# Optimization experiments

Hardware: AMD Instinct MI355X
Metric: run time of the kernel (lower is better)

## Reference

```python
import jax, jax.numpy as jnp
import numpy as np


def setup_inputs() -> dict:
    key = jax.random.key(0)
    k1, k2 = jax.random.split(key)
    B, S, D = 4, 8192, 1024
    x = jax.random.normal(k1, (B, S, D), dtype=jnp.float32)
    alpha = jax.random.uniform(k2, (B, S, D), dtype=jnp.float32)
    return {"x": x, "alpha": alpha}


def reference(x, alpha):
    # Linear recurrence h_t = alpha_t * h_{t-1} + x_t, computed as an
    # associative scan over the sequence axis (axis=1).
    def linear_combine(i, j):
        x_i, a_i = i
        x_j, a_j = j
        return (a_j * x_i + x_j, a_j * a_i)

    ys, _ = jax.lax.associative_scan(linear_combine, (x, alpha), axis=1)
    return ys
```

## Files before the change

### kernel.cpp

```cpp
#include <hip/hip_runtime.h>

constexpr int B    = 4;
constexpr int S    = 8192;
constexpr int D    = 1024;
constexpr int CB   = 64;
constexpr int L    = S / CB;
constexpr int D4   = D / 4;
constexpr int NBLK = B * CB;
constexpr int G    = 8;
constexpr int NG   = L / G;

typedef float nt_float4 __attribute__((ext_vector_type(4)));

__device__ __forceinline__ void ast(float* p, float v) {
    __hip_atomic_store(p, v, __ATOMIC_RELAXED, __HIP_MEMORY_SCOPE_AGENT);
}
__device__ __forceinline__ float ald(const float* p) {
    return __hip_atomic_load(p, __ATOMIC_RELAXED, __HIP_MEMORY_SCOPE_AGENT);
}

__device__ __forceinline__ void gridbar(int* bar) {
    __syncthreads();
    if (threadIdx.x == 0) {
        __hip_atomic_fetch_add(bar, 1, __ATOMIC_ACQ_REL, __HIP_MEMORY_SCOPE_AGENT);
        while (__hip_atomic_load(bar, __ATOMIC_RELAXED, __HIP_MEMORY_SCOPE_AGENT) < NBLK)
            __builtin_amdgcn_s_sleep(2);
        __threadfence();
    }
    __syncthreads();
}

__device__ __forceinline__ void issue_grp(const float4* __restrict__ x,
                                          const float4* __restrict__ a,
                                          long o, float4 (&bx)[G], float4 (&ba)[G]) {
    #pragma unroll
    for (int j = 0; j < G; ++j) {
        bx[j] = x[o + (long)j * D4];
        ba[j] = a[o + (long)j * D4];
    }
}

__global__ __launch_bounds__(256, 1) void scan_coop(const float4* __restrict__ x,
                                                    const float4* __restrict__ a,
                                                    float4* __restrict__ out,
                                                    float* __restrict__ Xagg,
                                                    float* __restrict__ Aagg,
                                                    float* __restrict__ Pref,
                                                    int* __restrict__ bars) {
    const int t   = threadIdx.x;
    const int bid = blockIdx.x;
    const int b   = bid >> 6;
    const int c   = bid & (CB - 1);
    const long base = ((long)(b * S + c * L)) * D4 + t;

    float4 bx0[G], ba0[G], bx1[G], ba1[G];

    float4 X = {0.f, 0.f, 0.f, 0.f};
    float4 A = {1.f, 1.f, 1.f, 1.f};
    issue_grp(x, a, base, bx0, ba0);
    #pragma unroll
    for (int g = 0; g < NG; g += 2) {
        issue_grp(x, a, base + (long)(g + 1) * G * D4, bx1, ba1);
        #pragma unroll
        for (int j = 0; j < G; ++j) {
            X.x = fmaf(ba0[j].x, X.x, bx0[j].x); A.x *= ba0[j].x;
            X.y = fmaf(ba0[j].y, X.y, bx0[j].y); A.y *= ba0[j].y;
            X.z = fmaf(ba0[j].z, X.z, bx0[j].z); A.z *= ba0[j].z;
            X.w = fmaf(ba0[j].w, X.w, bx0[j].w); A.w *= ba0[j].w;
        }
        if (g + 2 < NG) issue_grp(x, a, base + (long)(g + 2) * G * D4, bx0, ba0);
        #pragma unroll
        for (int j = 0; j < G; ++j) {
            X.x = fmaf(ba1[j].x, X.x, bx1[j].x); A.x *= ba1[j].x;
            X.y = fmaf(ba1[j].y, X.y, bx1[j].y); A.y *= ba1[j].y;
            X.z = fmaf(ba1[j].z, X.z, bx1[j].z); A.z *= ba1[j].z;
            X.w = fmaf(ba1[j].w, X.w, bx1[j].w); A.w *= ba1[j].w;
        }
    }
    {
        float* Xp = Xagg + (long)bid * D + 4 * t;
        float* Ap = Aagg + (long)bid * D + 4 * t;
        ast(Xp + 0, X.x); ast(Xp + 1, X.y); ast(Xp + 2, X.z); ast(Xp + 3, X.w);
        ast(Ap + 0, A.x); ast(Ap + 1, A.y); ast(Ap + 2, A.z); ast(Ap + 3, A.w);
    }

    gridbar(bars + 0);

    if (bid < 16) {
        const int gg = bid * 256 + t;
        const int sb = gg >> 10;
        const int d  = gg & (D - 1);
        const float* Xp = Xagg + (long)sb * CB * D + d;
        const float* Ap = Aagg + (long)sb * CB * D + d;
        float*       Pp = Pref + (long)sb * CB * D + d;
        float carry = 0.f;
        for (int cc = 0; cc < CB; cc += 8) {
            float xv[8], av[8];
            #pragma unroll
            for (int j = 0; j < 8; ++j) {
                xv[j] = ald(Xp + (long)(cc + j) * D);
                av[j] = ald(Ap + (long)(cc + j) * D);
            }
            #pragma unroll
            for (int j = 0; j < 8; ++j) {
                ast(Pp + (long)(cc + j) * D, carry);
                carry = fmaf(av[j], carry, xv[j]);
            }
        }
    }

    gridbar(bars + 1);

    float4 h;
    {
        const float* Pp = Pref + (long)bid * D + 4 * t;
        h.x = ald(Pp + 0); h.y = ald(Pp + 1); h.z = ald(Pp + 2); h.w = ald(Pp + 3);
    }
    nt_float4* ntout = (nt_float4*)out;
    issue_grp(x, a, base, bx0, ba0);
    #pragma unroll
    for (int g = 0; g < NG; g += 2) {
        issue_grp(x, a, base + (long)(g + 1) * G * D4, bx1, ba1);
        #pragma unroll
        for (int j = 0; j < G; ++j) {
            h.x = fmaf(ba0[j].x, h.x, bx0[j].x);
            h.y = fmaf(ba0[j].y, h.y, bx0[j].y);
            h.z = fmaf(ba0[j].z, h.z, bx0[j].z);
            h.w = fmaf(ba0[j].w, h.w, bx0[j].w);
            nt_float4 hv = {h.x, h.y, h.z, h.w};
            __builtin_nontemporal_store(hv, &ntout[base + (long)(g * G + j) * D4]);
        }
        if (g + 2 < NG) issue_grp(x, a, base + (long)(g + 2) * G * D4, bx0, ba0);
        #pragma unroll
        for (int j = 0; j < G; ++j) {
            h.x = fmaf(ba1[j].x, h.x, bx1[j].x);
            h.y = fmaf(ba1[j].y, h.y, bx1[j].y);
            h.z = fmaf(ba1[j].z, h.z, bx1[j].z);
            h.w = fmaf(ba1[j].w, h.w, bx1[j].w);
            nt_float4 hv = {h.x, h.y, h.z, h.w};
            __builtin_nontemporal_store(hv, &ntout[base + (long)((g + 1) * G + j) * D4]);
        }
    }
}

extern "C" void kernel_launch(void* const* d_in, const int* in_sizes, int n_in,
                              void* d_out, int out_size, void* d_ws, size_t ws_size,
                              hipStream_t stream) {
    const float4* x = (const float4*)d_in[0];
    const float4* a = (const float4*)d_in[1];
    float4* out = (float4*)d_out;

    char* ws = (char*)d_ws;
    int*   bars = (int*)ws;
    float* Xagg = (float*)(ws + 4096);
    float* Aagg = Xagg + (size_t)NBLK * D;
    float* Pref = Aagg + (size_t)NBLK * D;

    hipMemsetAsync(ws, 0, 4096, stream);
    scan_coop<<<dim3(NBLK), 256, 0, stream>>>(x, a, out, Xagg, Aagg, Pref, bars);
}
```

Measured before the change: 430.2 us.

## Split each block's chunk into two half-chunks scanned by two thread teams

```diff
diff --git a/kernel.cpp b/kernel.cpp
--- a/kernel.cpp
+++ b/kernel.cpp
@@ -5,10 +5,11 @@
 constexpr int D    = 1024;
 constexpr int CB   = 64;
 constexpr int L    = S / CB;
+constexpr int HL   = L / 2;
 constexpr int D4   = D / 4;
 constexpr int NBLK = B * CB;
 constexpr int G    = 8;
-constexpr int NG   = L / G;
+constexpr int NG   = HL / G;
 
 typedef float nt_float4 __attribute__((ext_vector_type(4)));
 
@@ -40,18 +41,22 @@
     }
 }
 
-__global__ __launch_bounds__(256, 1) void scan_coop(const float4* __restrict__ x,
+__global__ __launch_bounds__(512, 1) void scan_coop(const float4* __restrict__ x,
                                                     const float4* __restrict__ a,
                                                     float4* __restrict__ out,
                                                     float* __restrict__ Xagg,
                                                     float* __restrict__ Aagg,
                                                     float* __restrict__ Pref,
                                                     int* __restrict__ bars) {
-    const int t   = threadIdx.x;
-    const int bid = blockIdx.x;
-    const int b   = bid >> 6;
-    const int c   = bid & (CB - 1);
-    const long base = ((long)(b * S + c * L)) * D4 + t;
+    const int t    = threadIdx.x;
+    const int team = t >> 8;
+    const int u    = t & 255;
+    const int bid  = blockIdx.x;
+    const int b    = bid >> 6;
+    const int c    = bid & (CB - 1);
+    const long base = ((long)(b * S + c * L + team * HL)) * D4 + u;
+
+    __shared__ float4 lX0[256], lA0[256];
 
     float4 bx0[G], ba0[G], bx1[G], ba1[G];
 
@@ -77,16 +82,24 @@
             X.w = fmaf(ba1[j].w, X.w, bx1[j].w); A.w *= ba1[j].w;
         }
     }
-    {
-        float* Xp = Xagg + (long)bid * D + 4 * t;
-        float* Ap = Aagg + (long)bid * D + 4 * t;
-        ast(Xp + 0, X.x); ast(Xp + 1, X.y); ast(Xp + 2, X.z); ast(Xp + 3, X.w);
-        ast(Ap + 0, A.x); ast(Ap + 1, A.y); ast(Ap + 2, A.z); ast(Ap + 3, A.w);
+    if (team == 0) { lX0[u] = X; lA0[u] = A; }
+    __syncthreads();
+    if (team == 1) {
+        const float4 X0 = lX0[u], A0 = lA0[u];
+        float4 Xc, Ac;
+        Xc.x = fmaf(A.x, X0.x, X.x); Ac.x = A.x * A0.x;
+        Xc.y = fmaf(A.y, X0.y, X.y); Ac.y = A.y * A0.y;
+        Xc.z = fmaf(A.z, X0.z, X.z); Ac.z = A.z * A0.z;
+        Xc.w = fmaf(A.w, X0.w, X.w); Ac.w = A.w * A0.w;
+        float* Xp = Xagg + (long)bid * D + 4 * u;
+        float* Ap = Aagg + (long)bid * D + 4 * u;
+        ast(Xp + 0, Xc.x); ast(Xp + 1, Xc.y); ast(Xp + 2, Xc.z); ast(Xp + 3, Xc.w);
+        ast(Ap + 0, Ac.x); ast(Ap + 1, Ac.y); ast(Ap + 2, Ac.z); ast(Ap + 3, Ac.w);
     }
 
     gridbar(bars + 0);
 
-    if (bid < 16) {
+    if (bid < 16 && t < 256) {
         const int gg = bid * 256 + t;
         const int sb = gg >> 10;
         const int d  = gg & (D - 1);
@@ -113,8 +126,16 @@
 
     float4 h;
     {
-        const float* Pp = Pref + (long)bid * D + 4 * t;
-        h.x = ald(Pp + 0); h.y = ald(Pp + 1); h.z = ald(Pp + 2); h.w = ald(Pp + 3);
+        const float* Pp = Pref + (long)bid * D + 4 * u;
+        float4 cb;
+        cb.x = ald(Pp + 0); cb.y = ald(Pp + 1); cb.z = ald(Pp + 2); cb.w = ald(Pp + 3);
+        if (team == 0) h = cb;
+        else {
+            h.x = fmaf(lA0[u].x, cb.x, lX0[u].x);
+            h.y = fmaf(lA0[u].y, cb.y, lX0[u].y);
+            h.z = fmaf(lA0[u].z, cb.z, lX0[u].z);
+            h.w = fmaf(lA0[u].w, cb.w, lX0[u].w);
+        }
     }
     nt_float4* ntout = (nt_float4*)out;
     issue_grp(x, a, base, bx0, ba0);
@@ -157,5 +178,5 @@
     float* Pref = Aagg + (size_t)NBLK * D;
 
     hipMemsetAsync(ws, 0, 4096, stream);
-    scan_coop<<<dim3(NBLK), 256, 0, stream>>>(x, a, out, Xagg, Aagg, Pref, bars);
+    scan_coop<<<dim3(NBLK), 512, 0, stream>>>(x, a, out, Xagg, Aagg, Pref, bars);
 }
```

New measurement: 444.2 us. 3.3% more time.
